# Kernel tuning notes

Hardware: AMD Instinct MI355X
Metric: run time of the kernel (lower is better)

Reference implementation:

```python
import jax, jax.numpy as jnp
import numpy as np

SEQ_LEN = 2048   # configs.seq_len == h == KFSSM H
PRED_LEN = 720   # configs.pred_len == p
D_MODEL = 128    # configs.d_model == KFSSM N (complex state size N//2)
C_OUT = 64       # configs.c_out == channel dim of u
BATCH = 128


def setup_inputs() -> dict:
    key = jax.random.key(0)
    ks = jax.random.split(key, 12)
    H, n2, p = SEQ_LEN, D_MODEL // 2, PRED_LEN
    u = jax.random.normal(ks[0], (BATCH, SEQ_LEN, C_OUT), jnp.float32)
    x_mark_enc = jax.random.normal(ks[1], (BATCH, SEQ_LEN, 4), jnp.float32)
    x_dec = jax.random.normal(ks[2], (BATCH, PRED_LEN, C_OUT), jnp.float32)
    x_mark_dec = jax.random.normal(ks[3], (BATCH, PRED_LEN, 4), jnp.float32)
    # standard-normal noise; scaled by learned std inside reference (matches torch.normal(0, std))
    W_noise = jax.random.normal(ks[4], (BATCH, SEQ_LEN, C_OUT), jnp.float32)
    # Model params
    D = jax.random.normal(ks[5], (H,), jnp.float32)
    log_variance = jnp.log(1.0 + jax.random.uniform(ks[6], (1,), jnp.float32))
    # KFSSM params
    C_param = jax.random.normal(ks[7], (H, n2, 2), jnp.float32)  # view_as_real of complex C
    log_dt = (jax.random.uniform(ks[8], (H,), jnp.float32)
              * (np.log(0.1) - np.log(0.001)) + np.log(0.001))
    log_A_real = jnp.log(0.5 * jnp.ones((H, n2), jnp.float32))
    A_imag = np.pi * jnp.tile(jnp.arange(n2, dtype=jnp.float32)[None, :], (H, 1))
    # outporj: Linear(h -> 2p) then GLU(dim=2)
    proj_w = jax.random.normal(ks[9], (2 * p, H), jnp.float32) * 0.02
    proj_b = jnp.zeros((2 * p,), jnp.float32)
    return dict(u=u, x_mark_enc=x_mark_enc, x_dec=x_dec, x_mark_dec=x_mark_dec,
                W_noise=W_noise, D=D, log_variance=log_variance, C_param=C_param,
                log_dt=log_dt, log_A_real=log_A_real, A_imag=A_imag,
                proj_w=proj_w, proj_b=proj_b)


def _ssm_kernels(Nl, C_param, log_dt, log_A_real, A_imag):
    # KFSSM.forward(N=Nl): returns K, K2 of shape (H, Nl)
    dt = jnp.exp(log_dt)                              # (H,)
    C = C_param[..., 0] + 1j * C_param[..., 1]        # (H, n2)
    A = -jnp.exp(log_A_real) + 1j * A_imag            # (H, n2)
    ar = jnp.arange(Nl, dtype=log_dt.dtype)
    Bk = A[:, :1] * ar[None, :] * dt[:, None]         # (H, Nl) complex
    dtA = A * dt[:, None]                             # (H, n2)
    Kexp = jnp.exp(dtA[:, :, None] * ar[None, None, :])  # (H, n2, Nl)
    Cc = C * (jnp.exp(dtA) - 1.0) / A                 # (H, n2)
    K = 2.0 * jnp.einsum('hn,hnl->hl', Cc, Kexp).real # (H, Nl)
    K2 = 2.0 * (K * Bk).real                          # (H, Nl)
    return K, K2


def reference(u, x_mark_enc, x_dec, x_mark_dec, W_noise, D, log_variance,
              C_param, log_dt, log_A_real, A_imag, proj_w, proj_b):
    # instance normalization over time
    x_mean = jnp.mean(u, axis=1, keepdims=True)                  # (B,1,N)
    u0 = u - x_mean
    x_var = jnp.var(u0, axis=1, ddof=1, keepdims=True) + 1e-5    # unbiased, as torch.var
    un = u0 / jnp.sqrt(x_var)
    # Kalman process noise
    std = jnp.sqrt(jnp.exp(log_variance))                        # (1,)
    W = std * W_noise                                            # (B,L,N)
    l, Nch = un.shape[1], un.shape[2]
    nfft = 2 * l
    K, K2 = _ssm_kernels(Nch, C_param, log_dt, log_A_real, A_imag)  # (H=l, Nch)
    k_f = jnp.fft.rfft(K.T, n=nfft, axis=-1)                     # (Nch, l+1)
    k2_f = jnp.fft.rfft(K2.T, n=nfft, axis=-1)
    u_f = jnp.fft.rfft(jnp.transpose(un, (0, 2, 1)), n=nfft, axis=-1)   # (B,Nch,l+1)
    w_f = jnp.fft.rfft(jnp.transpose(W, (0, 2, 1)), n=nfft, axis=-1)
    y = (jnp.fft.irfft(u_f * k2_f, n=nfft, axis=-1)
         + jnp.fft.irfft(w_f * k_f, n=nfft, axis=-1))            # (B,Nch,2l)
    y = jnp.transpose(y, (0, 2, 1))[:, -l:, :] + un * D[:, None] # (B,l,Nch)
    # outporj: Linear(h->2p) over time axis, then GLU(dim=2); Dropout1d is identity at eval
    z = jnp.einsum('bnh,ph->bnp', jnp.transpose(y, (0, 2, 1)), proj_w) + proj_b  # (B,Nch,2p)
    a, b = jnp.split(z, 2, axis=2)
    y = jnp.transpose(a * jax.nn.sigmoid(b), (0, 2, 1))          # (B,p,Nch)
    y = y * jnp.sqrt(x_var) + x_mean
    return y[:, -PRED_LEN:, :]
```

## Files before the change

### kernel.cpp

```cpp
#include <hip/hip_runtime.h>
#include <math.h>

typedef unsigned short u16;
typedef __attribute__((ext_vector_type(8))) short short8;
typedef __attribute__((ext_vector_type(4))) float f32x4;

#define B_   128
#define L_   2048
#define C_   64
#define P_   720
#define P2_  1440
#define NPAD 1536
#define NFFT 4096
#define NROW (B_*C_)
#define TCHUNK 16

__device__ __forceinline__ u16 f2bf(float f) {
  union { float f; unsigned u; } x; x.f = f;
  unsigned r = x.u + 0x7fffu + ((x.u >> 16) & 1u);
  return (u16)(r >> 16);
}

__device__ __forceinline__ float2 cmul(float2 a, float2 b) {
  return make_float2(a.x * b.x - a.y * b.y, a.x * b.y + a.y * b.x);
}
__device__ __forceinline__ float2 cadd(float2 a, float2 b) { return make_float2(a.x + b.x, a.y + b.y); }
__device__ __forceinline__ float2 csub(float2 a, float2 b) { return make_float2(a.x - b.x, a.y - b.y); }

#define CSWAP(i, j) { float2 tt = a[i]; a[i] = a[j]; a[j] = tt; }

template<bool INV, bool HZ>
__device__ __forceinline__ void dft16(float2 a[16]) {
  const float S  = INV ? 1.f : -1.f;
  const float c1 = 0.9238795325112867f, s1 = 0.3826834323650898f, q2 = 0.7071067811865476f;
  const float2 W1 = make_float2( c1, S * s1), W2 = make_float2( q2, S * q2), W3 = make_float2( s1, S * c1);
  const float2 W5 = make_float2(-s1, S * c1), W6 = make_float2(-q2, S * q2), W7 = make_float2(-c1, S * s1);
  if (HZ) {
    a[8]  = a[0];
    a[9]  = cmul(a[1], W1);
    a[10] = cmul(a[2], W2);
    a[11] = cmul(a[3], W3);
    a[12] = make_float2(-S * a[4].y, S * a[4].x);
    a[13] = cmul(a[5], W5);
    a[14] = cmul(a[6], W6);
    a[15] = cmul(a[7], W7);
  } else {
    float2 t;
    t = csub(a[0], a[8]);  a[0] = cadd(a[0], a[8]);  a[8]  = t;
    t = csub(a[1], a[9]);  a[1] = cadd(a[1], a[9]);  a[9]  = cmul(t, W1);
    t = csub(a[2], a[10]); a[2] = cadd(a[2], a[10]); a[10] = cmul(t, W2);
    t = csub(a[3], a[11]); a[3] = cadd(a[3], a[11]); a[11] = cmul(t, W3);
    t = csub(a[4], a[12]); a[4] = cadd(a[4], a[12]); a[12] = make_float2(-S * t.y, S * t.x);
    t = csub(a[5], a[13]); a[5] = cadd(a[5], a[13]); a[13] = cmul(t, W5);
    t = csub(a[6], a[14]); a[6] = cadd(a[6], a[14]); a[14] = cmul(t, W6);
    t = csub(a[7], a[15]); a[7] = cadd(a[7], a[15]); a[15] = cmul(t, W7);
  }
#pragma unroll
  for (int h = 0; h < 16; h += 8) {
    float2 t;
    t = csub(a[h+0], a[h+4]); a[h+0] = cadd(a[h+0], a[h+4]); a[h+4] = t;
    t = csub(a[h+1], a[h+5]); a[h+1] = cadd(a[h+1], a[h+5]); a[h+5] = cmul(t, W2);
    t = csub(a[h+2], a[h+6]); a[h+2] = cadd(a[h+2], a[h+6]); a[h+6] = make_float2(-S * t.y, S * t.x);
    t = csub(a[h+3], a[h+7]); a[h+3] = cadd(a[h+3], a[h+7]); a[h+7] = cmul(t, W6);
  }
#pragma unroll
  for (int q = 0; q < 16; q += 4) {
    float2 t;
    t = csub(a[q+0], a[q+2]); a[q+0] = cadd(a[q+0], a[q+2]); a[q+2] = t;
    t = csub(a[q+1], a[q+3]); a[q+1] = cadd(a[q+1], a[q+3]); a[q+3] = make_float2(-S * t.y, S * t.x);
  }
#pragma unroll
  for (int p = 0; p < 16; p += 2) {
    float2 t = csub(a[p], a[p+1]); a[p] = cadd(a[p], a[p+1]); a[p+1] = t;
  }
  CSWAP(1, 8); CSWAP(2, 4); CSWAP(3, 12); CSWAP(5, 10); CSWAP(7, 14); CSWAP(11, 13);
}

__device__ __forceinline__ void twchain(float2 a[16], float2 w1) {
  float2 cur = w1;
  a[1] = cmul(a[1], cur);
#pragma unroll
  for (int k = 2; k < 16; ++k) { cur = cmul(cur, w1); a[k] = cmul(a[k], cur); }
}

__device__ __forceinline__ void lds_wA(float2* X, const float2 r[16], int tid) {
  int base = (tid & 15) * 16 + ((tid >> 4) ^ ((tid & 7) << 1));
#pragma unroll
  for (int i = 0; i < 16; ++i) X[base + i * 256] = r[i];
}
__device__ __forceinline__ void lds_wB(float2* X, const float2 r[16], int tid) {
#pragma unroll
  for (int i = 0; i < 16; ++i)
    X[((tid & 0xF0) + i) * 16 + ((tid & 15) ^ ((i & 7) << 1))] = r[i];
}
__device__ __forceinline__ void lds_rd(const float2* X, float2 r[16], int tid) {
  const float4* X4 = (const float4*)X;
#pragma unroll
  for (int p = 0; p < 8; ++p) {
    float4 v = X4[tid * 8 + (p ^ (tid & 7))];
    r[2 * p]     = make_float2(v.x, v.y);
    r[2 * p + 1] = make_float2(v.z, v.w);
  }
}

__device__ __forceinline__ void fft_fwd_hz(float2 r[16], float2* X, int tid, const float2* twg) {
  dft16<false, true>(r);
  twchain(r, twg[tid]);
  lds_wA(X, r, tid);
  __syncthreads();
  lds_rd(X, r, tid);
  dft16<false, false>(r);
  twchain(r, twg[(tid & 15) << 4]);
  __syncthreads();
  lds_wB(X, r, tid);
  __syncthreads();
  lds_rd(X, r, tid);
  dft16<false, false>(r);
}

__device__ __forceinline__ void fft_inv(float2 r[16], float2* X, int tid, const float2* twg) {
  dft16<true, false>(r);
  __syncthreads();
  lds_wB(X, r, tid);
  __syncthreads();
  lds_rd(X, r, tid);
  float2 wb = twg[(tid & 15) << 4];
  twchain(r, make_float2(wb.x, -wb.y));
  dft16<true, false>(r);
  __syncthreads();
  lds_wA(X, r, tid);
  __syncthreads();
  lds_rd(X, r, tid);
  float2 wa = twg[tid];
  twchain(r, make_float2(wa.x, -wa.y));
  dft16<true, false>(r);
}

__global__ void k_twfill(float2* __restrict__ tw) {
  int k = threadIdx.x;
  double ang = -2.0 * 3.14159265358979323846 * (double)k / 4096.0;
  tw[k] = make_float2((float)cos(ang), (float)sin(ang));
}

__global__ void k_wconv(const float* __restrict__ pw, u16* __restrict__ wb) {
  size_t idx = (size_t)blockIdx.x * 256 + threadIdx.x;
  int n = (int)(idx >> 11);
  int k = (int)(idx & 2047);
  float v = (n < P2_) ? pw[(size_t)n * L_ + k] : 0.0f;
  wb[idx] = f2bf(v);
}

__global__ __launch_bounds__(256) void k_stats1(const float* __restrict__ u, float* __restrict__ ps,
                                                float* __restrict__ pq) {
  int blk = blockIdx.x;
  int b = blk >> 4, q = blk & 15;
  int tid = threadIdx.x;
  int c4 = tid & 15, g = tid >> 4;
  const float4* u4 = (const float4*)(u + ((size_t)b * L_ + q * 128) * C_);
  float4 s = make_float4(0.f, 0.f, 0.f, 0.f), sq = s;
#pragma unroll
  for (int i = 0; i < 8; ++i) {
    float4 v = u4[(size_t)(g + 16 * i) * 16 + c4];
    s.x += v.x; s.y += v.y; s.z += v.z; s.w += v.w;
    sq.x += v.x * v.x; sq.y += v.y * v.y; sq.z += v.z * v.z; sq.w += v.w * v.w;
  }
  __shared__ float4 sb[16][16], qb[16][16];
  sb[g][c4] = s; qb[g][c4] = sq;
  __syncthreads();
  if (g == 0) {
    float4 S = sb[0][c4], Q = qb[0][c4];
#pragma unroll
    for (int k = 1; k < 16; ++k) {
      float4 a = sb[k][c4], d = qb[k][c4];
      S.x += a.x; S.y += a.y; S.z += a.z; S.w += a.w;
      Q.x += d.x; Q.y += d.y; Q.z += d.z; Q.w += d.w;
    }
    ((float4*)ps)[blk * 16 + c4] = S;
    ((float4*)pq)[blk * 16 + c4] = Q;
  }
}

__global__ __launch_bounds__(256) void k_stats2(const float* __restrict__ ps, const float* __restrict__ pq,
                                                float4* __restrict__ mv) {
  int gid = blockIdx.x * 256 + threadIdx.x;
  int b = gid >> 6, c = gid & 63;
  float S = 0.f, Q = 0.f;
#pragma unroll
  for (int q = 0; q < 16; ++q) {
    S += ps[(size_t)(b * 16 + q) * 64 + c];
    Q += pq[(size_t)(b * 16 + q) * 64 + c];
  }
  float mean = S * (1.0f / 2048.0f);
  float var = (Q - S * S * (1.0f / 2048.0f)) * (1.0f / 2047.0f) + 1e-5f;
  float sv = sqrtf(var);
  mv[gid] = make_float4(mean, sv, 1.0f / sv, 0.0f);
}

__global__ __launch_bounds__(256) void k_ssmk(const float* __restrict__ Cp, const float* __restrict__ ldt,
                                              const float* __restrict__ lAr, const float* __restrict__ Aim,
                                              float2* __restrict__ kz) {
  int gid = blockIdx.x * 256 + threadIdx.x;
  int h = gid & 2047;
  int j = gid >> 11;
  float dt = expf(ldt[h]);
  float accx = 0.f;
  float Ar0 = 0.f;
  for (int n = 0; n < 64; ++n) {
    float Ar = -expf(lAr[h * 64 + n]);
    float Ai = Aim[h * 64 + n];
    if (n == 0) Ar0 = Ar;
    float dAr = Ar * dt, dAi = Ai * dt;
    float er = expf(dAr);
    float s1, c1; sincosf(dAi, &s1, &c1);
    float emr = er * c1 - 1.0f, emi = er * s1;
    float inv = 1.0f / (Ar * Ar + Ai * Ai);
    float qr = (emr * Ar + emi * Ai) * inv;
    float qi = (emi * Ar - emr * Ai) * inv;
    float cr = Cp[(size_t)(h * 64 + n) * 2];
    float ci = Cp[(size_t)(h * 64 + n) * 2 + 1];
    float ccr = cr * qr - ci * qi;
    float cci = cr * qi + ci * qr;
    float ej = expf(dAr * (float)j);
    float sj, cj; sincosf(dAi * (float)j, &sj, &cj);
    accx += ccr * (ej * cj) - cci * (ej * sj);
  }
  float K = 2.0f * accx;
  float K2 = 2.0f * K * (Ar0 * (float)j * dt);
  kz[(size_t)j * L_ + h] = make_float2(K2, -K);
}

__global__ __launch_bounds__(256) void k_packT(const float* __restrict__ u, const float* __restrict__ Wn,
                                               const float* __restrict__ lv, const float4* __restrict__ mv,
                                               float2* __restrict__ zu) {
  int b = blockIdx.x >> 5;
  int t0 = (blockIdx.x & 31) << 6;
  int tid = threadIdx.x;
  float stdn = sqrtf(expf(lv[0]));
  __shared__ float2 tile[64][65];
  int c = tid & 63, r = tid >> 6;
  float4 m = mv[b * C_ + c];
#pragma unroll
  for (int i = 0; i < 16; ++i) {
    int t = t0 + i * 4 + r;
    size_t idx = ((size_t)b * L_ + t) * C_ + c;
    float uu = (u[idx] - m.x) * m.z;
    float ww = Wn[idx] * stdn;
    tile[i * 4 + r][c] = make_float2(uu, ww);
  }
  __syncthreads();
  int t = tid & 63, cb = tid >> 6;
#pragma unroll
  for (int i = 0; i < 16; ++i) {
    int c2 = i * 4 + cb;
    zu[((size_t)(b * C_ + c2)) * L_ + t0 + t] = tile[t][c2];
  }
}

__global__ __launch_bounds__(256) void k_fftk(const float2* __restrict__ kz, const float2* __restrict__ twg,
                                              float2* __restrict__ G) {
  __shared__ float2 X[NFFT];
  int j = blockIdx.x, tid = threadIdx.x;
  float2 r[16];
#pragma unroll
  for (int n2 = 0; n2 < 8; ++n2) r[n2] = kz[(size_t)j * L_ + n2 * 256 + tid];
  fft_fwd_hz(r, X, tid, twg);
  const float sc = 1.0f / 4096.0f;
#pragma unroll
  for (int k0 = 0; k0 < 16; ++k0)
    G[(size_t)j * NFFT + k0 * 256 + tid] = make_float2(r[k0].x * sc, r[k0].y * sc);
}

__global__ __launch_bounds__(256) void k_fftmain(const float2* __restrict__ zu, const float2* __restrict__ twg,
                                                 const float2* __restrict__ G, const float* __restrict__ Dv,
                                                 u16* __restrict__ yT) {
  __shared__ float2 X[NFFT];
  int row = blockIdx.x;
  int j = row & 63;
  int tid = threadIdx.x;
  float2 r[16];
  float usav[8];
#pragma unroll
  for (int n2 = 0; n2 < 8; ++n2) {
    r[n2] = zu[(size_t)row * L_ + n2 * 256 + tid];
    usav[n2] = r[n2].x;
  }
  fft_fwd_hz(r, X, tid, twg);
  const float2* Gj = G + (size_t)j * NFFT;
#pragma unroll
  for (int k0 = 0; k0 < 16; ++k0) r[k0] = cmul(r[k0], Gj[k0 * 256 + tid]);
  fft_inv(r, X, tid, twg);
#pragma unroll
  for (int n2 = 8; n2 < 16; ++n2) {
    int t = (n2 - 8) * 256 + tid;
    float yv = r[n2].x + usav[n2 - 8] * Dv[t];
    yT[(size_t)row * L_ + t] = f2bf(yv);
  }
}

__global__ __launch_bounds__(256) void k_gemm(const u16* __restrict__ A, const u16* __restrict__ B,
                                              float* __restrict__ Cmat) {
  __shared__ u16 As[128 * 32];
  __shared__ u16 Bs[128 * 32];
  const int K = L_, N = NPAD;
  int tid = threadIdx.x;
  int bm = blockIdx.x % 64, bn = blockIdx.x / 64;
  int wave = tid >> 6, lane = tid & 63;
  int wm = (wave >> 1) << 6, wn = (wave & 1) << 6;
  int lr = lane & 15, lk = lane >> 4;
  int trow = tid >> 2, tk = (tid & 3) << 3;
  const u16* Ag = A + (size_t)(bm * 128 + trow) * K + tk;
  const u16* Bg = B + (size_t)(bn * 128 + trow) * K + tk;
  f32x4 acc[4][4] = {};
  uint4 pa0 = *(const uint4*)(Ag);
  uint4 pa1 = *(const uint4*)(Ag + (size_t)64 * K);
  uint4 pb0 = *(const uint4*)(Bg);
  uint4 pb1 = *(const uint4*)(Bg + (size_t)64 * K);
  for (int kt = 0; kt < K; kt += 32) {
    __syncthreads();
    *(uint4*)&As[trow * 32 + tk] = pa0;
    *(uint4*)&As[(trow + 64) * 32 + tk] = pa1;
    *(uint4*)&Bs[trow * 32 + tk] = pb0;
    *(uint4*)&Bs[(trow + 64) * 32 + tk] = pb1;
    __syncthreads();
    if (kt + 32 < K) {
      pa0 = *(const uint4*)(Ag + kt + 32);
      pa1 = *(const uint4*)(Ag + (size_t)64 * K + kt + 32);
      pb0 = *(const uint4*)(Bg + kt + 32);
      pb1 = *(const uint4*)(Bg + (size_t)64 * K + kt + 32);
    }
    short8 af[4], bf[4];
#pragma unroll
    for (int i2 = 0; i2 < 4; ++i2) af[i2] = *(const short8*)&As[(wm + i2 * 16 + lr) * 32 + lk * 8];
#pragma unroll
    for (int j2 = 0; j2 < 4; ++j2) bf[j2] = *(const short8*)&Bs[(wn + j2 * 16 + lr) * 32 + lk * 8];
#pragma unroll
    for (int i2 = 0; i2 < 4; ++i2)
#pragma unroll
      for (int j2 = 0; j2 < 4; ++j2)
        acc[i2][j2] = __builtin_amdgcn_mfma_f32_16x16x32_bf16(af[i2], bf[j2], acc[i2][j2], 0, 0, 0);
  }
#pragma unroll
  for (int i2 = 0; i2 < 4; ++i2)
#pragma unroll
    for (int j2 = 0; j2 < 4; ++j2)
#pragma unroll
      for (int r = 0; r < 4; ++r)
        Cmat[(size_t)(bm * 128 + wm + i2 * 16 + lk * 4 + r) * N + bn * 128 + wn + j2 * 16 + lr] =
            acc[i2][j2][r];
}

__global__ __launch_bounds__(256) void k_epi(const float* __restrict__ z, const float* __restrict__ pb,
                                             const float4* __restrict__ mv, float* __restrict__ out) {
  int b = blockIdx.x / 23;
  int p0 = (blockIdx.x % 23) * 32;
  int tid = threadIdx.x;
  __shared__ float tile[64][33];
  int pp = tid & 31, ci = tid >> 5;
  for (int cc = ci; cc < 64; cc += 8) {
    int p = p0 + pp;
    float val = 0.f;
    if (p < P_) {
      size_t rowb = (size_t)(b * C_ + cc) * NPAD;
      float a = z[rowb + p] + pb[p];
      float g = z[rowb + P_ + p] + pb[P_ + p];
      float4 m = mv[b * C_ + cc];
      val = a * (1.0f / (1.0f + expf(-g))) * m.y + m.x;
    }
    tile[cc][pp] = val;
  }
  __syncthreads();
  int c2 = tid & 63, pi = tid >> 6;
  for (int q = pi; q < 32; q += 4) {
    int p = p0 + q;
    if (p < P_) out[((size_t)b * P_ + p) * C_ + c2] = tile[c2][q];
  }
}

extern "C" void kernel_launch(void* const* d_in, const int* in_sizes, int n_in,
                              void* d_out, int out_size, void* d_ws, size_t ws_size,
                              hipStream_t stream) {
  const float* u   = (const float*)d_in[0];
  const float* Wn  = (const float*)d_in[4];
  const float* Dv  = (const float*)d_in[5];
  const float* lv  = (const float*)d_in[6];
  const float* Cp  = (const float*)d_in[7];
  const float* ldt = (const float*)d_in[8];
  const float* lAr = (const float*)d_in[9];
  const float* Aim = (const float*)d_in[10];
  const float* pw  = (const float*)d_in[11];
  const float* pb  = (const float*)d_in[12];
  float* out = (float*)d_out;
  char* ws = (char*)d_ws;

  float2* tw = (float2*)(ws + 0);
  float4* mv = (float4*)(ws + (64 << 10));
  float2* G  = (float2*)(ws + (1 << 20));
  float2* kz = (float2*)(ws + (3 << 20));
  u16*    Wb = (u16*)   (ws + (4 << 20));
  float*  ps = (float*) (ws + (10 << 20));
  float*  pq = (float*) (ws + (10 << 20) + (512 << 10));
  u16*    yT = (u16*)   (ws + (16 << 20));
  float2* zu = (float2*)(ws + ((size_t)48 << 20));
  float*  zz = (float*) (ws + ((size_t)48 << 20));

  k_twfill<<<1, 256, 0, stream>>>(tw);
  k_wconv<<<(NPAD * L_) / 256, 256, 0, stream>>>(pw, Wb);
  k_stats1<<<B_ * TCHUNK, 256, 0, stream>>>(u, ps, pq);
  k_stats2<<<(B_ * C_) / 256, 256, 0, stream>>>(ps, pq, mv);
  k_ssmk<<<(C_ * L_) / 256, 256, 0, stream>>>(Cp, ldt, lAr, Aim, kz);
  k_packT<<<B_ * (L_ / 64), 256, 0, stream>>>(u, Wn, lv, mv, zu);
  k_fftk<<<C_, 256, 0, stream>>>(kz, tw, G);
  k_fftmain<<<NROW, 256, 0, stream>>>(zu, tw, G, Dv, yT);
  k_gemm<<<64 * (NPAD / 128), 256, 0, stream>>>(yT, Wb, zz);
  k_epi<<<B_ * 23, 256, 0, stream>>>(zz, pb, mv, out);
}
```

Baseline: 374.3 us.

## Pack FFT inputs as bf16, parallelize twiddle chain, swizzle GEMM blocks, fast exp

The intermediate zu buffer holding normalized input and scaled noise is stored as packed bf16 pairs instead of float2, halving traffic between the pack and FFT kernels. The serial twiddle-power chain is replaced by a tree of products to shorten the dependency chain. GEMM block indices are swizzled for better L2 reuse, and expf is swapped for __expf in two places. Rounding the FFT inputs to bf16 lowers accuracy, and zz is moved to a separate workspace region so it no longer aliases zu.

```diff
diff --git a/kernel.cpp b/kernel.cpp
--- a/kernel.cpp
+++ b/kernel.cpp
@@ -2,6 +2,7 @@
 #include <math.h>
 
 typedef unsigned short u16;
+typedef unsigned int u32;
 typedef __attribute__((ext_vector_type(8))) short short8;
 typedef __attribute__((ext_vector_type(4))) float f32x4;
 
@@ -19,6 +20,12 @@
   union { float f; unsigned u; } x; x.f = f;
   unsigned r = x.u + 0x7fffu + ((x.u >> 16) & 1u);
   return (u16)(r >> 16);
+}
+__device__ __forceinline__ float bf2f_lo(u32 v) {
+  union { unsigned u; float f; } x; x.u = v << 16; return x.f;
+}
+__device__ __forceinline__ float bf2f_hi(u32 v) {
+  union { unsigned u; float f; } x; x.u = v & 0xffff0000u; return x.f;
 }
 
 __device__ __forceinline__ float2 cmul(float2 a, float2 b) {
@@ -77,10 +84,25 @@
 }
 
 __device__ __forceinline__ void twchain(float2 a[16], float2 w1) {
-  float2 cur = w1;
-  a[1] = cmul(a[1], cur);
-#pragma unroll
-  for (int k = 2; k < 16; ++k) { cur = cmul(cur, w1); a[k] = cmul(a[k], cur); }
+  float2 w2 = cmul(w1, w1);
+  float2 w3 = cmul(w2, w1);
+  float2 w4 = cmul(w2, w2);
+  float2 w5 = cmul(w3, w2);
+  float2 w6 = cmul(w3, w3);
+  float2 w7 = cmul(w4, w3);
+  float2 w8 = cmul(w4, w4);
+  float2 w9 = cmul(w5, w4);
+  float2 w10 = cmul(w5, w5);
+  float2 w11 = cmul(w6, w5);
+  float2 w12 = cmul(w6, w6);
+  float2 w13 = cmul(w7, w6);
+  float2 w14 = cmul(w7, w7);
+  float2 w15 = cmul(w8, w7);
+  a[1]  = cmul(a[1],  w1);  a[2]  = cmul(a[2],  w2);  a[3]  = cmul(a[3],  w3);
+  a[4]  = cmul(a[4],  w4);  a[5]  = cmul(a[5],  w5);  a[6]  = cmul(a[6],  w6);
+  a[7]  = cmul(a[7],  w7);  a[8]  = cmul(a[8],  w8);  a[9]  = cmul(a[9],  w9);
+  a[10] = cmul(a[10], w10); a[11] = cmul(a[11], w11); a[12] = cmul(a[12], w12);
+  a[13] = cmul(a[13], w13); a[14] = cmul(a[14], w14); a[15] = cmul(a[15], w15);
 }
 
 __device__ __forceinline__ void lds_wA(float2* X, const float2 r[16], int tid) {
@@ -231,11 +253,11 @@
 
 __global__ __launch_bounds__(256) void k_packT(const float* __restrict__ u, const float* __restrict__ Wn,
                                                const float* __restrict__ lv, const float4* __restrict__ mv,
-                                               float2* __restrict__ zu) {
+                                               u32* __restrict__ zu) {
   int b = blockIdx.x >> 5;
   int t0 = (blockIdx.x & 31) << 6;
   int tid = threadIdx.x;
-  float stdn = sqrtf(expf(lv[0]));
+  float stdn = sqrtf(__expf(lv[0]));
   __shared__ float2 tile[64][65];
   int c = tid & 63, r = tid >> 6;
   float4 m = mv[b * C_ + c];
@@ -252,7 +274,8 @@
 #pragma unroll
   for (int i = 0; i < 16; ++i) {
     int c2 = i * 4 + cb;
-    zu[((size_t)(b * C_ + c2)) * L_ + t0 + t] = tile[t][c2];
+    float2 v = tile[t][c2];
+    zu[((size_t)(b * C_ + c2)) * L_ + t0 + t] = ((u32)f2bf(v.y) << 16) | (u32)f2bf(v.x);
   }
 }
 
@@ -270,7 +293,7 @@
     G[(size_t)j * NFFT + k0 * 256 + tid] = make_float2(r[k0].x * sc, r[k0].y * sc);
 }
 
-__global__ __launch_bounds__(256) void k_fftmain(const float2* __restrict__ zu, const float2* __restrict__ twg,
+__global__ __launch_bounds__(256) void k_fftmain(const u32* __restrict__ zu, const float2* __restrict__ twg,
                                                  const float2* __restrict__ G, const float* __restrict__ Dv,
                                                  u16* __restrict__ yT) {
   __shared__ float2 X[NFFT];
@@ -281,8 +304,10 @@
   float usav[8];
 #pragma unroll
   for (int n2 = 0; n2 < 8; ++n2) {
-    r[n2] = zu[(size_t)row * L_ + n2 * 256 + tid];
-    usav[n2] = r[n2].x;
+    u32 v = zu[(size_t)row * L_ + n2 * 256 + tid];
+    float uu = bf2f_lo(v), ww = bf2f_hi(v);
+    r[n2] = make_float2(uu, ww);
+    usav[n2] = uu;
   }
   fft_fwd_hz(r, X, tid, twg);
   const float2* Gj = G + (size_t)j * NFFT;
@@ -303,7 +328,9 @@
   __shared__ u16 Bs[128 * 32];
   const int K = L_, N = NPAD;
   int tid = threadIdx.x;
-  int bm = blockIdx.x % 64, bn = blockIdx.x / 64;
+  int bid = blockIdx.x;
+  int swz = (bid & 7) * 96 + (bid >> 3);
+  int bm = swz % 64, bn = swz / 64;
   int wave = tid >> 6, lane = tid & 63;
   int wm = (wave >> 1) << 6, wn = (wave & 1) << 6;
   int lr = lane & 15, lk = lane >> 4;
@@ -364,7 +391,7 @@
       float a = z[rowb + p] + pb[p];
       float g = z[rowb + P_ + p] + pb[P_ + p];
       float4 m = mv[b * C_ + cc];
-      val = a * (1.0f / (1.0f + expf(-g))) * m.y + m.x;
+      val = a * (1.0f / (1.0f + __expf(-g))) * m.y + m.x;
     }
     tile[cc][pp] = val;
   }
@@ -400,8 +427,8 @@
   float*  ps = (float*) (ws + (10 << 20));
   float*  pq = (float*) (ws + (10 << 20) + (512 << 10));
   u16*    yT = (u16*)   (ws + (16 << 20));
-  float2* zu = (float2*)(ws + ((size_t)48 << 20));
-  float*  zz = (float*) (ws + ((size_t)48 << 20));
+  u32*    zu = (u32*)   (ws + ((size_t)48 << 20));
+  float*  zz = (float*) (ws + ((size_t)112 << 20));
 
   k_twfill<<<1, 256, 0, stream>>>(tw);
   k_wconv<<<(NPAD * L_) / 256, 256, 0, stream>>>(pw, Wb);
```

Result: faster. 353.1 us (-5.7%).
